# Optimization experiments

Hardware: AMD Instinct MI355X
Metric: run time of the kernel (lower is better)

## Reference

```python
import jax, jax.numpy as jnp
import numpy as np

B, V, S, F, K = 8, 2048, 4, 64, 8
MAX_DIST = np.float32(np.finfo(np.float32).max)


def setup_inputs() -> dict:
    key = jax.random.key(0)
    k1, k2 = jax.random.split(key)
    coordinates = jax.random.normal(k1, (B, V, S), dtype=jnp.float32)
    features = jax.random.normal(k2, (B, V, F), dtype=jnp.float32)
    # per-event number of active vertices (float, compared against the raw mask)
    active_vertices = jnp.full((B, 1), 0.75 * V, dtype=jnp.float32)
    return {"coordinates": coordinates, "features": features,
            "active_vertices": active_vertices}


def reference(coordinates, features, active_vertices):
    # squared euclidean distance matrix: |x_i - x_j|^2 = -2 x_i.x_j + |x_i|^2 + |x_j|^2
    sub = -2.0 * jnp.einsum('bvs,bws->bvw', coordinates, coordinates)
    dot = jnp.sum(coordinates * coordinates, axis=2)  # [B, V]
    dist = jnp.abs(sub + dot[:, :, None] + dot[:, None, :])  # [B, V, V]

    # raw mask: max(row_idx, col_idx); vertex pair valid iff both < n_active
    r = jnp.arange(V)
    raw_mask = jnp.maximum(r[None, :], r[:, None]).astype(jnp.float32)  # [V, V]
    mask = raw_mask[None, :, :] < active_vertices[:, :, None]  # [B, V, V]
    dist = jnp.where(mask, dist, MAX_DIST)

    # top-k smallest distances (self at rank 0 is dropped)
    neg_ranked, idx = jax.lax.top_k(-dist, K)  # [B, V, K]
    neighbour_idx = idx[:, :, 1:]              # [B, V, K-1]
    neighbour_distances = -neg_ranked[:, :, 1:]

    # gather neighbour features per batch: [B, V, K-1, F]
    batch_idx = jnp.arange(B)[:, None, None]
    neighbour_features = features[batch_idx, neighbour_idx]
    return neighbour_distances, neighbour_features
```

## Files before the change

kernel.cpp:

```cpp
#include <hip/hip_runtime.h>
#include <cstdint>
#include <cfloat>
#include <cstddef>

#define BB 8
#define VV 2048
#define SS 4
#define FF 64
#define KK 8

#define BF16_SAFE_MAX 3.3e38f

typedef unsigned long long u64;
typedef unsigned int u32;

#define KEY_BIAS (1ULL << 62)

static __forceinline__ __device__ double mk_key(float d, u32 w) {
    return __longlong_as_double(
        (long long)(KEY_BIAS | ((u64)__float_as_uint(d) << 20) | (u64)w));
}
static __forceinline__ __device__ u32 key_dist(double k) {
    return (u32)(((u64)__double_as_longlong(k)) >> 20);
}
static __forceinline__ __device__ u32 key_idx(double k) {
    return (u32)((u64)__double_as_longlong(k) & (u64)(VV - 1));
}
static __forceinline__ __device__ double shfl_xor_f64(double x, int m) {
    const u64 b = (u64)__double_as_longlong(x);
    int lo = __shfl_xor((int)(u32)b, m, 64);
    int hi = __shfl_xor((int)(u32)(b >> 32), m, 64);
    return __longlong_as_double((long long)(((u64)(u32)hi << 32) | (u32)lo));
}

#define CED(A, x, y) { double lo_ = fmin(A[x], A[y]);                          \
                       double hi_ = fmax(A[x], A[y]);                          \
                       A[x] = lo_; A[y] = hi_; }

#define SORT8D(K, O)                                                           \
    CED(K,O+0,O+1) CED(K,O+2,O+3) CED(K,O+4,O+5) CED(K,O+6,O+7)                \
    CED(K,O+0,O+2) CED(K,O+1,O+3) CED(K,O+4,O+6) CED(K,O+5,O+7)                \
    CED(K,O+1,O+2) CED(K,O+5,O+6)                                              \
    CED(K,O+0,O+4) CED(K,O+1,O+5) CED(K,O+2,O+6) CED(K,O+3,O+7)                \
    CED(K,O+2,O+4) CED(K,O+3,O+5)                                              \
    CED(K,O+1,O+2) CED(K,O+3,O+4) CED(K,O+5,O+6)

#define CLEAN8D(t)                                                             \
    CED(t,0,4) CED(t,1,5) CED(t,2,6) CED(t,3,7)                                \
    CED(t,0,2) CED(t,1,3) CED(t,4,6) CED(t,5,7)                                \
    CED(t,0,1) CED(t,2,3) CED(t,4,5) CED(t,6,7)

#define MERGE8D(T, S) {                                                        \
    double t[KK];                                                              \
    t[0] = fmin(T[0], S[7]);  t[1] = fmin(T[1], S[6]);                         \
    t[2] = fmin(T[2], S[5]);  t[3] = fmin(T[3], S[4]);                         \
    t[4] = fmin(T[4], S[3]);  t[5] = fmin(T[5], S[2]);                         \
    t[6] = fmin(T[6], S[1]);  t[7] = fmin(T[7], S[0]);                         \
    CLEAN8D(t)                                                                 \
    T[0]=t[0]; T[1]=t[1]; T[2]=t[2]; T[3]=t[3];                                \
    T[4]=t[4]; T[5]=t[5]; T[6]=t[6]; T[7]=t[7]; }

__global__ __launch_bounds__(256, 6)
void knn_topk_kernel(const float* __restrict__ coords,
                     const float* __restrict__ feats,
                     const float* __restrict__ active,
                     float* __restrict__ out_dist,
                     float* __restrict__ out_feat)
{
#pragma clang fp contract(off)
    __shared__ float4 sc[VV / 2];
    __shared__ float  sn[VV / 2];

    const int b   = blockIdx.y;
    const int tid = threadIdx.x;
    const int l   = tid & 31;
    const int j   = tid >> 5;
    const int v   = blockIdx.x + (j << 8);

    const float A = active[b];
    int Ai = (int)ceilf(A);
    Ai = Ai < 0 ? 0 : (Ai > VV ? VV : Ai);

    const size_t row = (size_t)b * VV + v;
    const float4* cg = reinterpret_cast<const float4*>(coords + (size_t)b * VV * SS);

    const bool rowActive = ((float)v < A);
    const bool heavy = (__ballot(rowActive) != 0ULL);
    const int  Aieff = rowActive ? Ai : 0;

    const float4 cv = cg[v];
    float qp0 = cv.x*cv.x, qp1 = cv.y*cv.y, qp2 = cv.z*cv.z, qp3 = cv.w*cv.w;
    const float nv = ((qp0 + qp1) + qp2) + qp3;

    double top[KK];
#pragma unroll
    for (int i = 0; i < KK; ++i)
        top[i] = __longlong_as_double((long long)(KEY_BIAS | 0xFFFFFFFFFFFFFULL));

    int ntiles = (Ai + 31) >> 5;
    if (ntiles < 16) ntiles = 16;
    const int nb = (ntiles + 15) >> 4;
    const int nb1 = nb < 2 ? nb : 2;

#define STAGE(P)                                                               \
    for (int i = tid; i < VV / 2; i += 256) {                                  \
        const float4 c = cg[i + ((P) << 10)];                                  \
        float p0 = c.x*c.x, p1 = c.y*c.y, p2 = c.z*c.z, p3 = c.w*c.w;          \
        sn[i] = ((p0 + p1) + p2) + p3;                 \
        float4 c2;                                                             \
        c2.x = -2.0f*c.x; c2.y = -2.0f*c.y;                                    \
        c2.z = -2.0f*c.z; c2.w = -2.0f*c.w;                 \
        sc[i] = c2;                                                            \
    }

#define CAND_KEY(K, slot, T)                                                   \
    {                                                                          \
        const int w  = ((T) << 5) + l;                                         \
        const int wi = w & (VV / 2 - 1);                                       \
        const float4 cw = sc[wi];                                              \
        const float  nw = sn[wi];                                              \
        float q0 = cv.x*cw.x, q1 = cv.y*cw.y,                                  \
              q2 = cv.z*cw.z, q3 = cv.w*cw.w;                                  \
        float dotp = ((q0 + q1) + q2) + q3;                                    \
        float sd = dotp + nv;                                                  \
        sd = sd + nw;                                                          \
        sd = fabsf(sd);                                                        \
        const float dvf = (w < Aieff) ? sd : FLT_MAX;                          \
        K[slot] = mk_key(dvf, (u32)w);                                         \
    }

#define SCAN_BATCH(M)                                                          \
    {                                                                          \
        const int bt = (M) << 4;                                               \
        double bk[16];                                                         \
        _Pragma("unroll")                                                      \
        for (int k = 0; k < 16; ++k) CAND_KEY(bk, k, bt + k)                   \
        SORT8D(bk, 0)                                                          \
        SORT8D(bk, 8)                                                          \
        double s8[KK];                           \
        s8[0] = fmin(bk[0], bk[15]); s8[1] = fmin(bk[1], bk[14]);              \
        s8[2] = fmin(bk[2], bk[13]); s8[3] = fmin(bk[3], bk[12]);              \
        s8[4] = fmin(bk[4], bk[11]); s8[5] = fmin(bk[5], bk[10]);              \
        s8[6] = fmin(bk[6], bk[9]);  s8[7] = fmin(bk[7], bk[8]);               \
        CLEAN8D(s8)                                                            \
        MERGE8D(top, s8)                                                       \
    }

    STAGE(0)
    __syncthreads();
    if (heavy) {
        for (int m = 0; m < nb1; ++m) SCAN_BATCH(m)
    }

    if (nb > 2) {
        __syncthreads();
        STAGE(1)
        __syncthreads();
        if (heavy) {
            for (int m = 2; m < nb; ++m) SCAN_BATCH(m)
        }
    }
#undef STAGE
#undef CAND_KEY
#undef SCAN_BATCH

    if (!heavy) {
        if (l >= 1 && l < KK)
            out_dist[row * (KK - 1) + (l - 1)] = BF16_SAFE_MAX;
#pragma unroll
        for (int r = 1; r < KK; ++r) {
            const float2 val = reinterpret_cast<const float2*>(
                feats + ((size_t)b * VV + r) * FF)[l];
            reinterpret_cast<float2*>(out_feat + (row * (KK - 1) + (r - 1)) * FF)[l] = val;
        }
        return;
    }

#pragma unroll
    for (int step = 1; step < 32; step <<= 1) {
        double t[KK];
#pragma unroll
        for (int i = 0; i < KK; ++i) {
            double pb = shfl_xor_f64(top[KK - 1 - i], step);
            t[i] = fmin(top[i], pb);
        }
        CLEAN8D(t)
#pragma unroll
        for (int i = 0; i < KK; ++i) top[i] = t[i];
    }

    u32 kd = 0;
#pragma unroll
    for (int r = 1; r < KK; ++r) kd = (l == r) ? key_dist(top[r]) : kd;
    if (l >= 1 && l < KK) {
        float d = __uint_as_float(kd);
        if (!(d <= BF16_SAFE_MAX)) d = BF16_SAFE_MAX;
        out_dist[row * (KK - 1) + (l - 1)] = d;
    }

#pragma unroll
    for (int r = 1; r < KK; ++r) {
        const u32 idx = key_idx(top[r]);
        const float2 val = reinterpret_cast<const float2*>(
            feats + ((size_t)b * VV + idx) * FF)[l];
        reinterpret_cast<float2*>(out_feat + (row * (KK - 1) + (r - 1)) * FF)[l] = val;
    }
}

extern "C" void kernel_launch(void* const* d_in, const int* in_sizes, int n_in,
                              void* d_out, int out_size, void* d_ws, size_t ws_size,
                              hipStream_t stream)
{
    const float* coords = (const float*)d_in[0];
    const float* feats  = (const float*)d_in[1];
    const float* act    = (const float*)d_in[2];
    float* out_dist = (float*)d_out;
    float* out_feat = out_dist + (size_t)BB * VV * (KK - 1);

    dim3 grid(VV / 8, BB);
    knn_topk_kernel<<<grid, dim3(256), 0, stream>>>(coords, feats, act,
                                                    out_dist, out_feat);
}
```

Before: 28.43 us.

## Stage all coordinates in LDS once, fold masking into norms, nontemporal output stores

```diff
diff --git a/kernel.cpp b/kernel.cpp
--- a/kernel.cpp
+++ b/kernel.cpp
@@ -31,6 +31,10 @@
     int lo = __shfl_xor((int)(u32)b, m, 64);
     int hi = __shfl_xor((int)(u32)(b >> 32), m, 64);
     return __longlong_as_double((long long)(((u64)(u32)hi << 32) | (u32)lo));
+}
+static __forceinline__ __device__ void nt_store_f2(float* p, float2 v) {
+    union { float2 f; u64 u; } c; c.f = v;
+    __builtin_nontemporal_store(c.u, (u64*)p);
 }
 
 #define CED(A, x, y) { double lo_ = fmin(A[x], A[y]);                          \
@@ -60,7 +64,7 @@
     T[0]=t[0]; T[1]=t[1]; T[2]=t[2]; T[3]=t[3];                                \
     T[4]=t[4]; T[5]=t[5]; T[6]=t[6]; T[7]=t[7]; }
 
-__global__ __launch_bounds__(256, 6)
+__global__ __launch_bounds__(256, 4)
 void knn_topk_kernel(const float* __restrict__ coords,
                      const float* __restrict__ feats,
                      const float* __restrict__ active,
@@ -68,8 +72,8 @@
                      float* __restrict__ out_feat)
 {
 #pragma clang fp contract(off)
-    __shared__ float4 sc[VV / 2];
-    __shared__ float  sn[VV / 2];
+    __shared__ float4 sc[VV];
+    __shared__ float  sn[VV];
 
     const int b   = blockIdx.y;
     const int tid = threadIdx.x;
@@ -86,47 +90,44 @@
 
     const bool rowActive = ((float)v < A);
     const bool heavy = (__ballot(rowActive) != 0ULL);
-    const int  Aieff = rowActive ? Ai : 0;
 
     const float4 cv = cg[v];
     float qp0 = cv.x*cv.x, qp1 = cv.y*cv.y, qp2 = cv.z*cv.z, qp3 = cv.w*cv.w;
-    const float nv = ((qp0 + qp1) + qp2) + qp3;
+    const float nv  = ((qp0 + qp1) + qp2) + qp3;
+    const float nvp = rowActive ? nv : FLT_MAX;
 
     double top[KK];
 #pragma unroll
     for (int i = 0; i < KK; ++i)
         top[i] = __longlong_as_double((long long)(KEY_BIAS | 0xFFFFFFFFFFFFFULL));
 
-    int ntiles = (Ai + 31) >> 5;
-    if (ntiles < 16) ntiles = 16;
-    const int nb = (ntiles + 15) >> 4;
-    const int nb1 = nb < 2 ? nb : 2;
-
-#define STAGE(P)                                                               \
-    for (int i = tid; i < VV / 2; i += 256) {                                  \
-        const float4 c = cg[i + ((P) << 10)];                                  \
-        float p0 = c.x*c.x, p1 = c.y*c.y, p2 = c.z*c.z, p3 = c.w*c.w;          \
-        sn[i] = ((p0 + p1) + p2) + p3;                 \
-        float4 c2;                                                             \
-        c2.x = -2.0f*c.x; c2.y = -2.0f*c.y;                                    \
-        c2.z = -2.0f*c.z; c2.w = -2.0f*c.w;                 \
-        sc[i] = c2;                                                            \
-    }
-
-#define CAND_KEY(K, slot, T)                                                   \
-    {                                                                          \
-        const int w  = ((T) << 5) + l;                                         \
-        const int wi = w & (VV / 2 - 1);                                       \
-        const float4 cw = sc[wi];                                              \
-        const float  nw = sn[wi];                                              \
-        float q0 = cv.x*cw.x, q1 = cv.y*cw.y,                                  \
-              q2 = cv.z*cw.z, q3 = cv.w*cw.w;                                  \
-        float dotp = ((q0 + q1) + q2) + q3;                                    \
-        float sd = dotp + nv;                                                  \
-        sd = sd + nw;                                                          \
-        sd = fabsf(sd);                                                        \
-        const float dvf = (w < Aieff) ? sd : FLT_MAX;                          \
-        K[slot] = mk_key(dvf, (u32)w);                                         \
+    const int ntiles = (Ai + 31) >> 5;
+    int nb = (ntiles + 15) >> 4;
+    if (nb < 1) nb = 1;
+
+    for (int i = tid; i < VV; i += 256) {
+        const float4 c = cg[i];
+        float p0 = c.x*c.x, p1 = c.y*c.y, p2 = c.z*c.z, p3 = c.w*c.w;
+        const float nrm = ((p0 + p1) + p2) + p3;
+        sn[i] = (i < Ai) ? nrm : FLT_MAX;
+        float4 c2;
+        c2.x = -2.0f*c.x; c2.y = -2.0f*c.y;
+        c2.z = -2.0f*c.z; c2.w = -2.0f*c.w;
+        sc[i] = c2;
+    }
+    __syncthreads();
+
+    if (!heavy) {
+        if (l >= 1 && l < KK)
+            __builtin_nontemporal_store(BF16_SAFE_MAX,
+                                        &out_dist[row * (KK - 1) + (l - 1)]);
+#pragma unroll
+        for (int r = 1; r < KK; ++r) {
+            const float2 val = reinterpret_cast<const float2*>(
+                feats + ((size_t)b * VV + r) * FF)[l];
+            nt_store_f2(out_feat + (row * (KK - 1) + (r - 1)) * FF + 2 * l, val);
+        }
+        return;
     }
 
 #define SCAN_BATCH(M)                                                          \
@@ -134,7 +135,18 @@
         const int bt = (M) << 4;                                               \
         double bk[16];                                                         \
         _Pragma("unroll")                                                      \
-        for (int k = 0; k < 16; ++k) CAND_KEY(bk, k, bt + k)                   \
+        for (int k = 0; k < 16; ++k) {                                         \
+            const int w = ((bt + k) << 5) + l;                                 \
+            const float4 cw = sc[w];                                           \
+            const float  nw = sn[w];                                           \
+            float q0 = cv.x*cw.x, q1 = cv.y*cw.y,                              \
+                  q2 = cv.z*cw.z, q3 = cv.w*cw.w;                              \
+            float dotp = ((q0 + q1) + q2) + q3;         \
+            float sd = dotp + nvp;                                             \
+            sd = sd + nw;                                                      \
+            sd = fabsf(sd);                         \
+            bk[k] = mk_key(sd, (u32)w);                                        \
+        }                                                                      \
         SORT8D(bk, 0)                                                          \
         SORT8D(bk, 8)                                                          \
         double s8[KK];                           \
@@ -146,35 +158,8 @@
         MERGE8D(top, s8)                                                       \
     }
 
-    STAGE(0)
-    __syncthreads();
-    if (heavy) {
-        for (int m = 0; m < nb1; ++m) SCAN_BATCH(m)
-    }
-
-    if (nb > 2) {
-        __syncthreads();
-        STAGE(1)
-        __syncthreads();
-        if (heavy) {
-            for (int m = 2; m < nb; ++m) SCAN_BATCH(m)
-        }
-    }
-#undef STAGE
-#undef CAND_KEY
+    for (int m = 0; m < nb; ++m) SCAN_BATCH(m)
 #undef SCAN_BATCH
-
-    if (!heavy) {
-        if (l >= 1 && l < KK)
-            out_dist[row * (KK - 1) + (l - 1)] = BF16_SAFE_MAX;
-#pragma unroll
-        for (int r = 1; r < KK; ++r) {
-            const float2 val = reinterpret_cast<const float2*>(
-                feats + ((size_t)b * VV + r) * FF)[l];
-            reinterpret_cast<float2*>(out_feat + (row * (KK - 1) + (r - 1)) * FF)[l] = val;
-        }
-        return;
-    }
 
 #pragma unroll
     for (int step = 1; step < 32; step <<= 1) {
@@ -195,7 +180,7 @@
     if (l >= 1 && l < KK) {
         float d = __uint_as_float(kd);
         if (!(d <= BF16_SAFE_MAX)) d = BF16_SAFE_MAX;
-        out_dist[row * (KK - 1) + (l - 1)] = d;
+        __builtin_nontemporal_store(d, &out_dist[row * (KK - 1) + (l - 1)]);
     }
 
 #pragma unroll
@@ -203,7 +188,7 @@
         const u32 idx = key_idx(top[r]);
         const float2 val = reinterpret_cast<const float2*>(
             feats + ((size_t)b * VV + idx) * FF)[l];
-        reinterpret_cast<float2*>(out_feat + (row * (KK - 1) + (r - 1)) * FF)[l] = val;
+        nt_store_f2(out_feat + (row * (KK - 1) + (r - 1)) * FF + 2 * l, val);
     }
 }
 
```

Result: slower. 30.42 us (+7.0%).
